# Performance work log

Hardware: AMD Instinct MI355X
Metric: run time of the kernel (lower is better)

## Reference

```python
import jax, jax.numpy as jnp
import numpy as np

B, DIM, H, W = 32, 256, 64, 64
WIN, SHIFT, HEADS = 8, 4, 8
HEAD_DIM = DIM // HEADS
SCALE = HEAD_DIM ** -0.5
N = WIN * WIN


def _window_partition(x, ws):
    # x: (B, H, W, C) -> (B*nW, ws, ws, C)
    b, h, w, c = x.shape
    x = x.reshape(b, h // ws, ws, w // ws, ws, c)
    return x.transpose(0, 1, 3, 2, 4, 5).reshape(-1, ws, ws, c)


def _window_reverse(windows, ws, h, w):
    # windows: (B*nW, ws, ws, C) -> (B, H, W, C)
    b = windows.shape[0] // ((h // ws) * (w // ws))
    x = windows.reshape(b, h // ws, w // ws, ws, ws, -1)
    return x.transpose(0, 1, 3, 2, 4, 5).reshape(b, h, w, -1)


def _rel_pos_index(ws):
    coords = np.stack(np.meshgrid(np.arange(ws), np.arange(ws), indexing='ij'))  # (2,ws,ws)
    cf = coords.reshape(2, -1)
    rel = cf[:, :, None] - cf[:, None, :]  # (2,N,N)
    rel = rel.transpose(1, 2, 0)
    rel[:, :, 0] += ws - 1
    rel[:, :, 1] += ws - 1
    rel[:, :, 0] *= 2 * ws - 1
    return rel.sum(-1)  # (N,N) int


def _shift_mask(h, w, ws, shift):
    img_mask = np.zeros((1, h, w, 1), np.float32)
    slices = (slice(0, -ws), slice(-ws, -shift), slice(-shift, None))
    cnt = 0
    for hs in slices:
        for wsl in slices:
            img_mask[:, hs, wsl, :] = cnt
            cnt += 1
    mw = np.asarray(_window_partition(jnp.asarray(img_mask), ws)).reshape(-1, ws * ws)
    am = mw[:, None, :] - mw[:, :, None]  # (nW, N, N)
    return jnp.asarray(np.where(am != 0, -100.0, 0.0).astype(np.float32))


_REL_IDX = jnp.asarray(_rel_pos_index(WIN).reshape(-1))  # (N*N,)
_ATTN_MASK = _shift_mask(H, W, WIN, SHIFT)  # (nW, N, N)


def setup_inputs() -> dict:
    key = jax.random.key(0)
    k1, k2, k3, k4 = jax.random.split(key, 4)
    x = jax.random.normal(k1, (B, DIM, H, W), jnp.float32)
    qkv_w = jax.random.normal(k2, (DIM, 3 * DIM), jnp.float32) * (DIM ** -0.5)
    qkv_b = jax.random.normal(k3, (3 * DIM,), jnp.float32) * 0.02
    rel_bias_table = jax.random.normal(k4, ((2 * WIN - 1) ** 2, HEADS), jnp.float32) * 0.02
    return {"x": x, "qkv_w": qkv_w, "qkv_b": qkv_b, "rel_bias_table": rel_bias_table}


def reference(x, qkv_w, qkv_b, rel_bias_table):
    b, c, h, w = x.shape
    xp = x.transpose(0, 2, 3, 1)  # (B,H,W,C)
    xs = jnp.roll(xp, (-SHIFT, -SHIFT), axis=(1, 2))
    win = _window_partition(xs, WIN).reshape(-1, N, c)  # (BW,N,C)
    bw = win.shape[0]
    qkv = win @ qkv_w + qkv_b  # (BW,N,3C)
    qkv = qkv.reshape(bw, N, 3, HEADS, HEAD_DIM).transpose(2, 0, 3, 1, 4)
    q, k, v = qkv[0], qkv[1], qkv[2]  # (BW,heads,N,hd)
    attn = jnp.einsum('whnd,whmd->whnm', q * SCALE, k)  # (BW,heads,N,N)
    bias = rel_bias_table[_REL_IDX].reshape(N, N, HEADS).transpose(2, 0, 1)  # (heads,N,N)
    attn = attn + bias[None]
    n_win = _ATTN_MASK.shape[0]
    attn = attn.reshape(b, n_win, HEADS, N, N) + _ATTN_MASK[None, :, None]
    attn = jax.nn.softmax(attn.reshape(bw, HEADS, N, N), axis=-1)
    out = jnp.einsum('whnm,whmd->whnd', attn, v)  # (BW,heads,N,hd)
    out = out.transpose(0, 2, 1, 3).reshape(bw, N, DIM)
    out = out.reshape(-1, WIN, WIN, DIM)
    out = _window_reverse(out, WIN, h, w)  # (B,H,W,C)
    out = jnp.roll(out, (SHIFT, SHIFT), axis=(1, 2))
    return out.transpose(0, 3, 1, 2)  # (B,C,H,W)
```

## Files before the change

kernel.cpp:

```cpp
#include <hip/hip_runtime.h>


typedef __attribute__((ext_vector_type(8))) short short8;
typedef __attribute__((ext_vector_type(4))) float f32x4;

static __device__ __forceinline__ short f2bf(float f) {
    unsigned u = __float_as_uint(f);
    u = (u + 0x7fffu + ((u >> 16) & 1u)) >> 16;
    return (short)u;
}

static __device__ __forceinline__ int region(int i) {
    return (i < 56) ? 0 : ((i < 60) ? 1 : 2);
}

static __device__ __forceinline__ void barrier_lds() {
    asm volatile("s_waitcnt lgkmcnt(0)" ::: "memory");
    __builtin_amdgcn_s_barrier();
    asm volatile("" ::: "memory");
}

static __device__ __forceinline__ float dpp_max16(float x) {
    float t;
    t = __int_as_float(__builtin_amdgcn_update_dpp(__float_as_int(x), __float_as_int(x), 0xB1, 0xF, 0xF, true));
    x = fmaxf(x, t);
    t = __int_as_float(__builtin_amdgcn_update_dpp(__float_as_int(x), __float_as_int(x), 0x4E, 0xF, 0xF, true));
    x = fmaxf(x, t);
    t = __int_as_float(__builtin_amdgcn_update_dpp(__float_as_int(x), __float_as_int(x), 0x141, 0xF, 0xF, true));
    x = fmaxf(x, t);
    t = __int_as_float(__builtin_amdgcn_update_dpp(__float_as_int(x), __float_as_int(x), 0x140, 0xF, 0xF, true));
    x = fmaxf(x, t);
    return x;
}

static __device__ __forceinline__ float dpp_sum16(float x) {
    float t;
    t = __int_as_float(__builtin_amdgcn_update_dpp(__float_as_int(x), __float_as_int(x), 0xB1, 0xF, 0xF, true));
    x += t;
    t = __int_as_float(__builtin_amdgcn_update_dpp(__float_as_int(x), __float_as_int(x), 0x4E, 0xF, 0xF, true));
    x += t;
    t = __int_as_float(__builtin_amdgcn_update_dpp(__float_as_int(x), __float_as_int(x), 0x141, 0xF, 0xF, true));
    x += t;
    t = __int_as_float(__builtin_amdgcn_update_dpp(__float_as_int(x), __float_as_int(x), 0x140, 0xF, 0xF, true));
    x += t;
    return x;
}

__global__ __launch_bounds__(256) void wt_transpose(const float* __restrict__ w,
                                                    unsigned short* __restrict__ wt) {
    __shared__ unsigned short t[64][72];
    int bx = blockIdx.x;
    int by = blockIdx.y;
    int tx = threadIdx.x & 63;
    int ty = threadIdx.x >> 6;
    #pragma unroll
    for (int i = 0; i < 16; ++i) {
        int k = i * 4 + ty;
        t[k][tx] = (unsigned short)f2bf(w[(by * 64 + k) * 768 + bx * 64 + tx]);
    }
    __syncthreads();
    #pragma unroll
    for (int i = 0; i < 16; ++i) {
        int c = i * 4 + ty;
        wt[(size_t)(bx * 64 + c) * 256 + by * 64 + tx] = t[tx][c];
    }
}

__global__ __launch_bounds__(512)
__attribute__((amdgpu_waves_per_eu(4, 4)))
void swin_kernel(
    const float* __restrict__ x,
    const unsigned short* __restrict__ wt,
    const float* __restrict__ qkv_b,
    const float* __restrict__ tbl,
    float* __restrict__ out)
{
    __shared__ char smem[80384];
    unsigned short* w_s = (unsigned short*)(smem);

    const int tid  = threadIdx.x;
    const int wave = tid >> 6;
    const int lane = tid & 63;
    const int ln   = lane & 15;
    const int quad = lane >> 4;
    const int win  = wave >> 2;
    const int wv   = wave & 3;

    const int blk = ((blockIdx.x & 7) << 7) + (blockIdx.x >> 3);
    const int b   = blk >> 5;
    const int wh  = (blk >> 2) & 7;
    const int wp  = blk & 3;
    const int ww  = wp * 2 + win;

    unsigned short* q_s  = (unsigned short*)(smem + 50688 + win * 14848);
    unsigned short* k_s  = (unsigned short*)(smem + 50688 + win * 14848 + 5120);
    unsigned short* vt_s = (unsigned short*)(smem + 50688 + win * 14848 + 10240);
    unsigned short* p_s  = (unsigned short*)(smem + win * 17664);

    const int t_a  = wv * 16 + ln;
    const int ti_a = t_a >> 3, tj_a = t_a & 7;
    const int si = (wh * 8 + ti_a + 4) & 63;
    const int sj = (ww * 8 + tj_a + 4) & 63;
    const float* xb = x + ((size_t)b * 256) * 4096 + si * 64 + sj;
    short8 afrag[8];
    #pragma unroll
    for (int ks = 0; ks < 8; ++ks) {
        #pragma unroll
        for (int j = 0; j < 8; ++j) {
            int c = ks * 32 + quad * 8 + j;
            afrag[ks][j] = f2bf(xb[(size_t)c * 4096]);
        }
    }

    const int row0 = wv * 16 + quad * 4;

    unsigned mmask = 0;
    unsigned idxp[4];
    #pragma unroll
    for (int nt = 0; nt < 4; ++nt) {
        int tk = nt * 16 + ln;
        int tik = tk >> 3, tjk = tk & 7;
        int cntk = region(wh * 8 + tik) * 3 + region(ww * 8 + tjk);
        unsigned pk = 0;
        #pragma unroll
        for (int r = 0; r < 4; ++r) {
            int tq = row0 + r;
            int tiq = tq >> 3, tjq = tq & 7;
            int idx = (tiq - tik + 7) * 15 + (tjq - tjk + 7);
            pk |= (unsigned)idx << (8 * r);
            int cntq = region(wh * 8 + tiq) * 3 + region(ww * 8 + tjq);
            if (cntq != cntk) mmask |= 1u << (nt * 4 + r);
        }
        idxp[nt] = pk;
    }

    const int di_o  = (wh * 8 + wv * 2 + (quad >> 1) + 4) & 63;
    const int dj_o  = (ww * 8 + (quad & 1) * 4 + 4) & 63;

    short8 wpre[6];
    #pragma unroll
    for (int i = 0; i < 6; ++i) {
        int idx = i * 512 + tid;
        int cl  = idx >> 5;
        int ch  = idx & 31;
        int col = ((cl >> 5) << 8) + (cl & 31);
        wpre[i] = *(const short8*)(wt + col * 256 + ch * 8);
    }

    for (int h = 0; h < 8; ++h) {
        barrier_lds();

        #pragma unroll
        for (int i = 0; i < 6; ++i) {
            int idx = i * 512 + tid;
            int cl  = idx >> 5;
            int ch  = idx & 31;
            *(short8*)(w_s + cl * 264 + ch * 8) = wpre[i];
        }
        barrier_lds();

        f32x4 acc[6];
        #pragma unroll
        for (int jt = 0; jt < 6; ++jt) acc[jt] = (f32x4){0.f, 0.f, 0.f, 0.f};
        #pragma unroll
        for (int ks = 0; ks < 8; ++ks) {
            short8 a = afrag[ks];
            #pragma unroll
            for (int jt = 0; jt < 6; ++jt) {
                short8 bb = *(const short8*)(w_s + (jt * 16 + ln) * 264 + ks * 32 + quad * 8);
                acc[jt] = __builtin_amdgcn_mfma_f32_16x16x32_bf16(a, bb, acc[jt], 0, 0, 0);
            }
        }

        if (h < 7) {
            #pragma unroll
            for (int i = 0; i < 6; ++i) {
                int idx = i * 512 + tid;
                int cl  = idx >> 5;
                int ch  = idx & 31;
                int col = ((cl >> 5) << 8) + ((h + 1) << 5) + (cl & 31);
                wpre[i] = *(const short8*)(wt + col * 256 + ch * 8);
            }
        }

        #pragma unroll
        for (int jt = 0; jt < 6; ++jt) {
            int colL = jt * 16 + ln;
            int seg  = colL >> 5;
            int cc   = colL & 31;
            float bias = qkv_b[(seg << 8) + (h << 5) + cc];
            #pragma unroll
            for (int r = 0; r < 4; ++r) {
                float v = acc[jt][r] + bias;
                int tok = row0 + r;
                if (seg == 0)      q_s[tok * 40 + cc] = (unsigned short)f2bf(v * 0.17677669529663689f);
                else if (seg == 1) k_s[tok * 40 + cc] = (unsigned short)f2bf(v);
                else               vt_s[cc * 72 + tok] = (unsigned short)f2bf(v);
            }
        }
        barrier_lds();

        short8 aq = *(const short8*)(q_s + (wv * 16 + ln) * 40 + quad * 8);
        f32x4 sacc[4];
        #pragma unroll
        for (int nt = 0; nt < 4; ++nt) {
            short8 bk = *(const short8*)(k_s + (nt * 16 + ln) * 40 + quad * 8);
            f32x4 z = (f32x4){0.f, 0.f, 0.f, 0.f};
            sacc[nt] = __builtin_amdgcn_mfma_f32_16x16x32_bf16(aq, bk, z, 0, 0, 0);
        }
        float sv[4][4];
        #pragma unroll
        for (int nt = 0; nt < 4; ++nt) {
            #pragma unroll
            for (int r = 0; r < 4; ++r) {
                int idx = (idxp[nt] >> (8 * r)) & 255;
                float s = sacc[nt][r] + tbl[idx * 8 + h];
                s += ((mmask >> (nt * 4 + r)) & 1) ? -100.0f : 0.0f;
                sv[nt][r] = s;
            }
        }
        #pragma unroll
        for (int r = 0; r < 4; ++r) {
            float m = fmaxf(fmaxf(sv[0][r], sv[1][r]), fmaxf(sv[2][r], sv[3][r]));
            m = dpp_max16(m);
            float p0 = __expf(sv[0][r] - m);
            float p1 = __expf(sv[1][r] - m);
            float p2 = __expf(sv[2][r] - m);
            float p3 = __expf(sv[3][r] - m);
            float ssum = dpp_sum16(p0 + p1 + p2 + p3);
            float inv = __builtin_amdgcn_rcpf(ssum);
            int pr = (row0 + r) * 72;
            p_s[pr +      ln] = (unsigned short)f2bf(p0 * inv);
            p_s[pr + 16 + ln] = (unsigned short)f2bf(p1 * inv);
            p_s[pr + 32 + ln] = (unsigned short)f2bf(p2 * inv);
            p_s[pr + 48 + ln] = (unsigned short)f2bf(p3 * inv);
        }

        f32x4 oacc[2];
        oacc[0] = (f32x4){0.f, 0.f, 0.f, 0.f};
        oacc[1] = (f32x4){0.f, 0.f, 0.f, 0.f};
        #pragma unroll
        for (int ks = 0; ks < 2; ++ks) {
            short8 ap = *(const short8*)(p_s + (wv * 16 + ln) * 72 + ks * 32 + quad * 8);
            #pragma unroll
            for (int nt = 0; nt < 2; ++nt) {
                short8 bv = *(const short8*)(vt_s + (nt * 16 + ln) * 72 + ks * 32 + quad * 8);
                oacc[nt] = __builtin_amdgcn_mfma_f32_16x16x32_bf16(ap, bv, oacc[nt], 0, 0, 0);
            }
        }

        #pragma unroll
        for (int nt = 0; nt < 2; ++nt) {
            int c = (h << 5) + nt * 16 + ln;
            float* op = out + ((size_t)(b * 256 + c)) * 4096 + di_o * 64 + dj_o;
            *(f32x4*)op = oacc[nt];
        }
    }
}

extern "C" void kernel_launch(void* const* d_in, const int* in_sizes, int n_in,
                              void* d_out, int out_size, void* d_ws, size_t ws_size,
                              hipStream_t stream) {
    const float* x      = (const float*)d_in[0];
    const float* qkv_w  = (const float*)d_in[1];
    const float* qkv_b  = (const float*)d_in[2];
    const float* tbl    = (const float*)d_in[3];
    float* out          = (float*)d_out;
    unsigned short* Wt  = (unsigned short*)d_ws;

    wt_transpose<<<dim3(12, 4), dim3(256), 0, stream>>>(qkv_w, Wt);
    swin_kernel<<<dim3(1024), dim3(512), 0, stream>>>(x, Wt, qkv_b, tbl, out);
}
```

Measured before the change: 513.2 us.

## Halve weight staging tile and shrink LDS footprint to raise occupancy

```diff
diff --git a/kernel.cpp b/kernel.cpp
--- a/kernel.cpp
+++ b/kernel.cpp
@@ -67,7 +67,7 @@
 }
 
 __global__ __launch_bounds__(512)
-__attribute__((amdgpu_waves_per_eu(4, 4)))
+__attribute__((amdgpu_waves_per_eu(6)))
 void swin_kernel(
     const float* __restrict__ x,
     const unsigned short* __restrict__ wt,
@@ -75,7 +75,7 @@
     const float* __restrict__ tbl,
     float* __restrict__ out)
 {
-    __shared__ char smem[80384];
+    __shared__ char smem[53760];
     unsigned short* w_s = (unsigned short*)(smem);
 
     const int tid  = threadIdx.x;
@@ -92,10 +92,9 @@
     const int wp  = blk & 3;
     const int ww  = wp * 2 + win;
 
-    unsigned short* q_s  = (unsigned short*)(smem + 50688 + win * 14848);
-    unsigned short* k_s  = (unsigned short*)(smem + 50688 + win * 14848 + 5120);
-    unsigned short* vt_s = (unsigned short*)(smem + 50688 + win * 14848 + 10240);
-    unsigned short* p_s  = (unsigned short*)(smem + win * 17664);
+    unsigned short* qk_s = (unsigned short*)(smem + 26112 + win * 13824);
+    unsigned short* vt_s = (unsigned short*)(smem + 26112 + win * 13824 + 9216);
+    unsigned short* p_s  = (unsigned short*)(smem + win * 9216);
 
     const int t_a  = wv * 16 + ln;
     const int ti_a = t_a >> 3, tj_a = t_a & 7;
@@ -137,49 +136,55 @@
     const int di_o  = (wh * 8 + wv * 2 + (quad >> 1) + 4) & 63;
     const int dj_o  = (ww * 8 + (quad & 1) * 4 + 4) & 63;
 
-    short8 wpre[6];
-    #pragma unroll
-    for (int i = 0; i < 6; ++i) {
+    short8 wpre[3];
+    #pragma unroll
+    for (int i = 0; i < 3; ++i) {
         int idx = i * 512 + tid;
-        int cl  = idx >> 5;
-        int ch  = idx & 31;
+        int cl  = idx >> 4;
+        int ch  = idx & 15;
         int col = ((cl >> 5) << 8) + (cl & 31);
         wpre[i] = *(const short8*)(wt + col * 256 + ch * 8);
     }
 
     for (int h = 0; h < 8; ++h) {
-        barrier_lds();
-
-        #pragma unroll
-        for (int i = 0; i < 6; ++i) {
-            int idx = i * 512 + tid;
-            int cl  = idx >> 5;
-            int ch  = idx & 31;
-            *(short8*)(w_s + cl * 264 + ch * 8) = wpre[i];
-        }
-        barrier_lds();
-
         f32x4 acc[6];
         #pragma unroll
         for (int jt = 0; jt < 6; ++jt) acc[jt] = (f32x4){0.f, 0.f, 0.f, 0.f};
-        #pragma unroll
-        for (int ks = 0; ks < 8; ++ks) {
-            short8 a = afrag[ks];
-            #pragma unroll
-            for (int jt = 0; jt < 6; ++jt) {
-                short8 bb = *(const short8*)(w_s + (jt * 16 + ln) * 264 + ks * 32 + quad * 8);
-                acc[jt] = __builtin_amdgcn_mfma_f32_16x16x32_bf16(a, bb, acc[jt], 0, 0, 0);
-            }
-        }
-
-        if (h < 7) {
-            #pragma unroll
-            for (int i = 0; i < 6; ++i) {
+
+        #pragma unroll
+        for (int half = 0; half < 2; ++half) {
+            barrier_lds();
+
+            #pragma unroll
+            for (int i = 0; i < 3; ++i) {
                 int idx = i * 512 + tid;
-                int cl  = idx >> 5;
-                int ch  = idx & 31;
-                int col = ((cl >> 5) << 8) + ((h + 1) << 5) + (cl & 31);
-                wpre[i] = *(const short8*)(wt + col * 256 + ch * 8);
+                int cl  = idx >> 4;
+                int ch  = idx & 15;
+                *(short8*)(w_s + cl * 136 + ch * 8) = wpre[i];
+            }
+            barrier_lds();
+
+            if (half == 0 || h < 7) {
+                int nh    = (half == 0) ? h : h + 1;
+                int nhalf = half ^ 1;
+                #pragma unroll
+                for (int i = 0; i < 3; ++i) {
+                    int idx = i * 512 + tid;
+                    int cl  = idx >> 4;
+                    int ch  = idx & 15;
+                    int col = ((cl >> 5) << 8) + (nh << 5) + (cl & 31);
+                    wpre[i] = *(const short8*)(wt + col * 256 + nhalf * 128 + ch * 8);
+                }
+            }
+
+            #pragma unroll
+            for (int ks2 = 0; ks2 < 4; ++ks2) {
+                short8 a = afrag[half * 4 + ks2];
+                #pragma unroll
+                for (int jt = 0; jt < 6; ++jt) {
+                    short8 bb = *(const short8*)(w_s + (jt * 16 + ln) * 136 + ks2 * 32 + quad * 8);
+                    acc[jt] = __builtin_amdgcn_mfma_f32_16x16x32_bf16(a, bb, acc[jt], 0, 0, 0);
+                }
             }
         }
 
@@ -193,18 +198,18 @@
             for (int r = 0; r < 4; ++r) {
                 float v = acc[jt][r] + bias;
                 int tok = row0 + r;
-                if (seg == 0)      q_s[tok * 40 + cc] = (unsigned short)f2bf(v * 0.17677669529663689f);
-                else if (seg == 1) k_s[tok * 40 + cc] = (unsigned short)f2bf(v);
-                else               vt_s[cc * 72 + tok] = (unsigned short)f2bf(v);
+                if (seg == 0)      qk_s[tok * 72 + cc]      = (unsigned short)f2bf(v * 0.17677669529663689f);
+                else if (seg == 1) qk_s[tok * 72 + 32 + cc] = (unsigned short)f2bf(v);
+                else               vt_s[cc * 72 + tok]      = (unsigned short)f2bf(v);
             }
         }
         barrier_lds();
 
-        short8 aq = *(const short8*)(q_s + (wv * 16 + ln) * 40 + quad * 8);
+        short8 aq = *(const short8*)(qk_s + (wv * 16 + ln) * 72 + quad * 8);
         f32x4 sacc[4];
         #pragma unroll
         for (int nt = 0; nt < 4; ++nt) {
-            short8 bk = *(const short8*)(k_s + (nt * 16 + ln) * 40 + quad * 8);
+            short8 bk = *(const short8*)(qk_s + (nt * 16 + ln) * 72 + 32 + quad * 8);
             f32x4 z = (f32x4){0.f, 0.f, 0.f, 0.f};
             sacc[nt] = __builtin_amdgcn_mfma_f32_16x16x32_bf16(aq, bk, z, 0, 0, 0);
         }
```

New measurement: 879.9 us. +71.4%, slower.
